# Performance work log

Hardware: AMD Instinct MI355X
Metric: run time of the kernel (lower is better)

## Reference

```python
import jax, jax.numpy as jnp
import numpy as np

B, Q, S, H = 2048, 128, 128, 32  # batch, num slices, slice length, hidden dim
C = Q * S


def setup_inputs() -> dict:
    key = jax.random.key(0)
    k0, k1, k2 = jax.random.split(key, 3)
    x = jax.random.normal(k0, (B, 1, 1, C), dtype=jnp.float32)
    # stacked per-slice MLP params (Glorot-ish scaling)
    W1 = jax.random.normal(k1, (Q, S, H), dtype=jnp.float32) * (1.0 / np.sqrt(S))
    b1 = jnp.zeros((Q, H), dtype=jnp.float32)
    W2 = jax.random.normal(k2, (Q, H, 1), dtype=jnp.float32) * (1.0 / np.sqrt(H))
    b2 = jnp.zeros((Q, 1), dtype=jnp.float32)
    return {"x": x, "W1": W1, "b1": b1, "W2": W2, "b2": b2}


def reference(x, W1, b1, W2, b2):
    # (B,1,1,C) -> (B,Q,S): slice the channel dim into Q groups
    xs = x.reshape(x.shape[0], Q, -1)
    # per-slice Dense(H) with ELU: grouped GEMM over the Q axis
    h = jax.nn.elu(jnp.einsum("bqs,qsh->bqh", xs, W1) + b1)  # (B,Q,H)
    # per-slice Dense(1): contract hidden dim -> scalar per slice
    out = jnp.einsum("bqh,qh->bq", h, W2[..., 0]) + b2[..., 0]  # (B,Q)
    return out
```

## Files before the change

kernel.cpp:

```cpp
#include <hip/hip_runtime.h>
#include <hip/hip_bf16.h>
#include <math.h>

#define QN 128
#define SN 128
#define HN 32
#define CN (QN * SN)
#define TILE_R 256

using half8   = __attribute__((ext_vector_type(8))) _Float16;
using floatx4 = __attribute__((ext_vector_type(4))) float;

__global__ __launch_bounds__(256, 4)
void divenc_kernel(const float* __restrict__ x,
                   const float* __restrict__ W1,
                   const float* __restrict__ b1,
                   const float* __restrict__ W2,
                   const float* __restrict__ b2,
                   float* __restrict__ out) {
  const int q    = blockIdx.x;
  const int b0   = blockIdx.y * TILE_R;
  const int tid  = threadIdx.x;
  const int lane = tid & 63;
  const int wid  = __builtin_amdgcn_readfirstlane(tid >> 6);
  const int nA   = lane & 15;
  const int koct = lane >> 4;

  const float* __restrict__ w1q = W1 + (size_t)q * (SN * HN);
  half8 bf[2][4];
  #pragma unroll
  for (int n0 = 0; n0 < 2; ++n0) {
    #pragma unroll
    for (int kk = 0; kk < 4; ++kk) {
      #pragma unroll
      for (int i = 0; i < 8; ++i) {
        const int k = kk * 32 + koct * 8 + i;
        bf[n0][kk][i] = (_Float16)w1q[k * HN + n0 * 16 + nA];
      }
    }
  }

  const float b1a = b1[q * HN + nA],  b1b = b1[q * HN + 16 + nA];
  const float w2a = W2[q * HN + nA],  w2b = W2[q * HN + 16 + nA];
  const float b2q = b2[q];

  const int row0 = b0 + wid * 64;
  const floatx4 z = {0.f, 0.f, 0.f, 0.f};

  #pragma unroll
  for (int mt = 0; mt < 4; ++mt) {
    floatx4 acc0 = z, acc1 = z;
    const float* __restrict__ rp =
        x + (size_t)(row0 + mt * 16 + nA) * CN + q * SN + koct * 8;
    #pragma unroll
    for (int kk = 0; kk < 4; ++kk) {
      const float4 va = *reinterpret_cast<const float4*>(rp + kk * 32);
      const float4 vb = *reinterpret_cast<const float4*>(rp + kk * 32 + 4);
      half8 af;
      af[0] = (_Float16)va.x; af[1] = (_Float16)va.y;
      af[2] = (_Float16)va.z; af[3] = (_Float16)va.w;
      af[4] = (_Float16)vb.x; af[5] = (_Float16)vb.y;
      af[6] = (_Float16)vb.z; af[7] = (_Float16)vb.w;
      acc0 = __builtin_amdgcn_mfma_f32_16x16x32_f16(af, bf[0][kk], acc0, 0, 0, 0);
      acc1 = __builtin_amdgcn_mfma_f32_16x16x32_f16(af, bf[1][kk], acc1, 0, 0, 0);
    }

    #pragma unroll
    for (int reg = 0; reg < 4; ++reg) {
      float v0 = acc0[reg] + b1a;
      v0 = v0 > 0.f ? v0 : expm1f(v0);
      float v1 = acc1[reg] + b1b;
      v1 = v1 > 0.f ? v1 : expm1f(v1);
      float t = fmaf(v0, w2a, v1 * w2b);
      t += __shfl_xor(t, 1);
      t += __shfl_xor(t, 2);
      t += __shfl_xor(t, 4);
      t += __shfl_xor(t, 8);
      if (nA == 0) {
        const int row = row0 + mt * 16 + koct * 4 + reg;
        out[(size_t)row * QN + q] = t + b2q;
      }
    }
  }
}

extern "C" void kernel_launch(void* const* d_in, const int* in_sizes, int n_in,
                              void* d_out, int out_size, void* d_ws, size_t ws_size,
                              hipStream_t stream) {
  const float* x  = (const float*)d_in[0];
  const float* W1 = (const float*)d_in[1];
  const float* b1 = (const float*)d_in[2];
  const float* W2 = (const float*)d_in[3];
  const float* b2 = (const float*)d_in[4];
  float* out = (float*)d_out;

  const int B = in_sizes[0] / CN;
  dim3 grid(QN, B / TILE_R);
  divenc_kernel<<<grid, 256, 0, stream>>>(x, W1, b1, W2, b2, out);
}
```

Measured before the change: 30.37 us.

## Shrink row tile to one MFMA tile per wave and use fast exp in ELU

Each wave now handles a single 16-row tile instead of four, and the block row tile drops from 256 to 64, giving four times as many blocks with a higher occupancy hint. W1 fragments are loaded inside the k loop instead of being preloaded for reuse across row tiles, so each block re-reads W1 for fewer rows. ELU now uses __expf minus one instead of expm1f, which is cheaper but less accurate near zero. The goal is more parallelism and memory-level concurrency for this bandwidth-bound read of x, paid for with more redundant W1 loads.

```diff
diff --git a/kernel.cpp b/kernel.cpp
--- a/kernel.cpp
+++ b/kernel.cpp
@@ -6,12 +6,12 @@
 #define SN 128
 #define HN 32
 #define CN (QN * SN)
-#define TILE_R 256
+#define TILE_R 64
 
 using half8   = __attribute__((ext_vector_type(8))) _Float16;
 using floatx4 = __attribute__((ext_vector_type(4))) float;
 
-__global__ __launch_bounds__(256, 4)
+__global__ __launch_bounds__(256, 8)
 void divenc_kernel(const float* __restrict__ x,
                    const float* __restrict__ W1,
                    const float* __restrict__ b1,
@@ -27,59 +27,54 @@
   const int koct = lane >> 4;
 
   const float* __restrict__ w1q = W1 + (size_t)q * (SN * HN);
-  half8 bf[2][4];
+  const int row0 = b0 + wid * 16;
+
+  floatx4 acc0 = {0.f, 0.f, 0.f, 0.f};
+  floatx4 acc1 = {0.f, 0.f, 0.f, 0.f};
+
+  const float* __restrict__ rp =
+      x + (size_t)(row0 + nA) * CN + q * SN + koct * 8;
+
   #pragma unroll
-  for (int n0 = 0; n0 < 2; ++n0) {
+  for (int kk = 0; kk < 4; ++kk) {
+    const float4 va = *reinterpret_cast<const float4*>(rp + kk * 32);
+    const float4 vb = *reinterpret_cast<const float4*>(rp + kk * 32 + 4);
+    half8 af;
+    af[0] = (_Float16)va.x; af[1] = (_Float16)va.y;
+    af[2] = (_Float16)va.z; af[3] = (_Float16)va.w;
+    af[4] = (_Float16)vb.x; af[5] = (_Float16)vb.y;
+    af[6] = (_Float16)vb.z; af[7] = (_Float16)vb.w;
+
+    half8 bf0, bf1;
     #pragma unroll
-    for (int kk = 0; kk < 4; ++kk) {
-      #pragma unroll
-      for (int i = 0; i < 8; ++i) {
-        const int k = kk * 32 + koct * 8 + i;
-        bf[n0][kk][i] = (_Float16)w1q[k * HN + n0 * 16 + nA];
-      }
+    for (int i = 0; i < 8; ++i) {
+      const int k = kk * 32 + koct * 8 + i;
+      bf0[i] = (_Float16)w1q[k * HN + nA];
+      bf1[i] = (_Float16)w1q[k * HN + 16 + nA];
     }
+
+    acc0 = __builtin_amdgcn_mfma_f32_16x16x32_f16(af, bf0, acc0, 0, 0, 0);
+    acc1 = __builtin_amdgcn_mfma_f32_16x16x32_f16(af, bf1, acc1, 0, 0, 0);
   }
 
   const float b1a = b1[q * HN + nA],  b1b = b1[q * HN + 16 + nA];
   const float w2a = W2[q * HN + nA],  w2b = W2[q * HN + 16 + nA];
   const float b2q = b2[q];
 
-  const int row0 = b0 + wid * 64;
-  const floatx4 z = {0.f, 0.f, 0.f, 0.f};
-
   #pragma unroll
-  for (int mt = 0; mt < 4; ++mt) {
-    floatx4 acc0 = z, acc1 = z;
-    const float* __restrict__ rp =
-        x + (size_t)(row0 + mt * 16 + nA) * CN + q * SN + koct * 8;
-    #pragma unroll
-    for (int kk = 0; kk < 4; ++kk) {
-      const float4 va = *reinterpret_cast<const float4*>(rp + kk * 32);
-      const float4 vb = *reinterpret_cast<const float4*>(rp + kk * 32 + 4);
-      half8 af;
-      af[0] = (_Float16)va.x; af[1] = (_Float16)va.y;
-      af[2] = (_Float16)va.z; af[3] = (_Float16)va.w;
-      af[4] = (_Float16)vb.x; af[5] = (_Float16)vb.y;
-      af[6] = (_Float16)vb.z; af[7] = (_Float16)vb.w;
-      acc0 = __builtin_amdgcn_mfma_f32_16x16x32_f16(af, bf[0][kk], acc0, 0, 0, 0);
-      acc1 = __builtin_amdgcn_mfma_f32_16x16x32_f16(af, bf[1][kk], acc1, 0, 0, 0);
-    }
-
-    #pragma unroll
-    for (int reg = 0; reg < 4; ++reg) {
-      float v0 = acc0[reg] + b1a;
-      v0 = v0 > 0.f ? v0 : expm1f(v0);
-      float v1 = acc1[reg] + b1b;
-      v1 = v1 > 0.f ? v1 : expm1f(v1);
-      float t = fmaf(v0, w2a, v1 * w2b);
-      t += __shfl_xor(t, 1);
-      t += __shfl_xor(t, 2);
-      t += __shfl_xor(t, 4);
-      t += __shfl_xor(t, 8);
-      if (nA == 0) {
-        const int row = row0 + mt * 16 + koct * 4 + reg;
-        out[(size_t)row * QN + q] = t + b2q;
-      }
+  for (int reg = 0; reg < 4; ++reg) {
+    float v0 = acc0[reg] + b1a;
+    v0 = v0 > 0.f ? v0 : (__expf(v0) - 1.f);
+    float v1 = acc1[reg] + b1b;
+    v1 = v1 > 0.f ? v1 : (__expf(v1) - 1.f);
+    float t = fmaf(v0, w2a, v1 * w2b);
+    t += __shfl_xor(t, 1);
+    t += __shfl_xor(t, 2);
+    t += __shfl_xor(t, 4);
+    t += __shfl_xor(t, 8);
+    if (nA == 0) {
+      const int row = row0 + koct * 4 + reg;
+      out[(size_t)row * QN + q] = t + b2q;
     }
   }
 }
```

Result: slower. 31.42 us (+3.5%).
